# Performance work log

Hardware: AMD Instinct MI355X
Metric: run time of the kernel (lower is better)

## Reference

```python
import jax, jax.numpy as jnp
import numpy as np

K = 16

def _knn_idx(pts, k):
    # pts: [B, 3, N] -> idx [B, N, k] (self-inclusive nearest neighbors)
    inner = -2.0 * jnp.einsum('bdn,bdm->bnm', pts, pts)
    xx = jnp.sum(pts * pts, axis=1)  # [B, N]
    pd = -xx[:, :, None] - inner - xx[:, None, :]  # negative squared distance
    _, idx = jax.lax.top_k(pd, k)
    return idx

def _gather(feats, idx):
    # feats: [B, N, D], idx: [B, N, k] -> [B, N, k, D]
    return jax.vmap(lambda f, i: f[i])(feats, idx)

def _conv1x1(x, w, b):
    # x: [B, Cin, N], w: [Cout, Cin], b: [Cout]
    return jnp.einsum('oi,bin->bon', w, x) + b[None, :, None]

def _linear(x, w, b):
    # x: [B, N, Din], w: [Dout, Din]
    return jnp.einsum('bnd,od->bno', x, w) + b

def _local_cov(pts, idx):
    # pts: [B, 3, N] -> [B, 12, N]
    nb = _gather(jnp.swapaxes(pts, 1, 2), idx)  # [B, N, k, 3]
    outer = nb[:, :, 0, :, None] * nb[:, :, 1, None, :]  # [B, N, 3, 3]
    B, N = pts.shape[0], pts.shape[2]
    outer = jnp.swapaxes(outer.reshape(B, N, 9), 1, 2)  # [B, 9, N]
    return jnp.concatenate([pts, outer], axis=1)

def _local_maxpool(x, idx):
    # x: [B, D, N] -> [B, N, D]
    nb = _gather(jnp.swapaxes(x, 1, 2), idx)  # [B, N, k, D]
    return jnp.max(nb, axis=2)

def setup_inputs() -> dict:
    key = jax.random.key(0)
    ks = jax.random.split(key, 20)
    def w(k, shape):
        return jax.random.normal(k, shape, dtype=jnp.float32) * 0.05
    pts = jax.random.normal(ks[0], (8, 3, 4096), dtype=jnp.float32)
    return {
        'pts': pts,
        'm1w1': w(ks[1], (64, 12)), 'm1b1': w(ks[2], (64,)),
        'm1w2': w(ks[3], (64, 64)), 'm1b2': w(ks[4], (64,)),
        'm1w3': w(ks[5], (64, 64)), 'm1b3': w(ks[6], (64,)),
        'l1w': w(ks[7], (64, 64)), 'l1b': w(ks[8], (64,)),
        'c1w': w(ks[9], (128, 64)), 'c1b': w(ks[10], (128,)),
        'l2w': w(ks[11], (128, 128)), 'l2b': w(ks[12], (128,)),
        'c2w': w(ks[13], (1024, 128)), 'c2b': w(ks[14], (1024,)),
        'm2w1': w(ks[15], (512, 1024)), 'm2b1': w(ks[16], (512,)),
        'm2w2': w(ks[17], (512, 512)), 'm2b2': w(ks[18], (512,)),
    }

def reference(pts, m1w1, m1b1, m1w2, m1b2, m1w3, m1b3, l1w, l1b,
              c1w, c1b, l2w, l2b, c2w, c2b, m2w1, m2b1, m2w2, m2b2):
    idx = _knn_idx(pts, K)  # [B, N, k]
    x = _local_cov(pts, idx)  # [B, 12, N]
    # mlp1: three 1x1 convs with ReLU
    x = jax.nn.relu(_conv1x1(x, m1w1, m1b1))
    x = jax.nn.relu(_conv1x1(x, m1w2, m1b2))
    x = jax.nn.relu(_conv1x1(x, m1w3, m1b3))  # [B, 64, N]
    # graph layer
    x = _local_maxpool(x, idx)          # [B, N, 64]
    x = _linear(x, l1w, l1b)            # [B, N, 64]
    x = jnp.swapaxes(x, 1, 2)           # [B, 64, N]
    x = jax.nn.relu(_conv1x1(x, c1w, c1b))  # [B, 128, N]
    x = _local_maxpool(x, idx)          # [B, N, 128]
    x = _linear(x, l2w, l2b)            # [B, N, 128]
    x = jnp.swapaxes(x, 1, 2)           # [B, 128, N]
    x = _conv1x1(x, c2w, c2b)           # [B, 1024, N]
    # global max pool
    x = jnp.max(x, axis=2, keepdims=True)  # [B, 1024, 1]
    # mlp2
    x = jax.nn.relu(_conv1x1(x, m2w1, m2b1))
    x = _conv1x1(x, m2w2, m2b2)  # [B, 512, 1]
    return x.reshape(-1, 512)
```

## Files before the change

kernel.cpp:

```cpp
#include <hip/hip_runtime.h>
#include <cfloat>

#define NBATCH 8
#define NPTS   4096
#define KNN    16
#define PPB    16
#define NSL    16
#define CAP    24

typedef unsigned short u16;
typedef unsigned int   u32;
typedef __attribute__((ext_vector_type(8))) short short8;
typedef __attribute__((ext_vector_type(4))) float f32x4;

__device__ __forceinline__ float relu_f(float x) { return x > 0.f ? x : 0.f; }

__device__ __forceinline__ u32 bf16_split_pack(float v)
{
    unsigned u = __float_as_uint(v);
    unsigned hb = (u + 0x7FFFu + ((u >> 16) & 1u)) >> 16;
    float hf = __uint_as_float(hb << 16);
    float l = v - hf;
    unsigned ul = __float_as_uint(l);
    unsigned lb = (ul + 0x7FFFu + ((ul >> 16) & 1u)) >> 16;
    return (hb << 16) | (lb & 0xFFFFu);
}

__device__ __forceinline__ void unpack8(uint4 a, uint4 b, short8& h, short8& l)
{
    union { unsigned u[4]; short8 s; } H, L;
    H.u[0] = __builtin_amdgcn_perm(a.y, a.x, 0x07060302);
    H.u[1] = __builtin_amdgcn_perm(a.w, a.z, 0x07060302);
    H.u[2] = __builtin_amdgcn_perm(b.y, b.x, 0x07060302);
    H.u[3] = __builtin_amdgcn_perm(b.w, b.z, 0x07060302);
    L.u[0] = __builtin_amdgcn_perm(a.y, a.x, 0x05040100);
    L.u[1] = __builtin_amdgcn_perm(a.w, a.z, 0x05040100);
    L.u[2] = __builtin_amdgcn_perm(b.y, b.x, 0x05040100);
    L.u[3] = __builtin_amdgcn_perm(b.w, b.z, 0x05040100);
    h = H.s; l = L.s;
}

__global__ __launch_bounds__(256)
void knn_kernel(const float* __restrict__ pts, int* __restrict__ idxout)
{
    __shared__ __align__(16) float4 tile[8 * 129];
    __shared__ float  kl[PPB * NSL * 8];
    __shared__ float  thr[PPB];
    __shared__ int    cnt[PPB];

    const int b = blockIdx.y, tid = threadIdx.x;
    const int ptl = tid >> 4, r = tid & 15;
    const int n = blockIdx.x * PPB + ptl;
    const float* pb = pts + (size_t)b * 3 * NPTS;

    const float sx = pb[n], sy = pb[NPTS + n], sz = pb[2 * NPTS + n];

    float k8[8];
#pragma unroll
    for (int s = 0; s < 8; ++s) k8[s] = -FLT_MAX;

    const float4* slice = tile + (r >> 1) * 129 + (r & 1) * 64;

    for (int t = 0; t < 4; ++t) {
        if (t) __syncthreads();
        for (int i = tid; i < 1024; i += 256) {
            int j = t * 1024 + i;
            float x = pb[j], y = pb[NPTS + j], z = pb[2 * NPTS + j];
            float xx = __fadd_rn(__fadd_rn(__fmul_rn(x, x), __fmul_rn(y, y)),
                                 __fmul_rn(z, z));
            tile[(i >> 7) * 129 + (i & 127)] = make_float4(x, y, z, xx);
        }
        __syncthreads();
#pragma unroll 8
        for (int ii = 0; ii < 64; ++ii) {
            float4 c = slice[ii];
            float dt = __fmaf_rn(sx, c.x, __fmaf_rn(sy, c.y, __fmul_rn(sz, c.z)));
            float pd = __fmaf_rn(2.f, dt, -c.w);
            float old0 = k8[0];
#pragma unroll
            for (int s = 7; s >= 1; --s)
                k8[s] = __builtin_amdgcn_fmed3f(k8[s - 1], k8[s], pd);
            k8[0] = fmaxf(old0, pd);
        }
    }

#pragma unroll
    for (int s = 0; s < 8; ++s) kl[(ptl * NSL + r) * 8 + s] = k8[s];
    __syncthreads();

    if (r == 0) {
        const float* L = kl + ptl * (NSL * 8);
        int p[NSL];
#pragma unroll
        for (int l = 0; l < NSL; ++l) p[l] = 0;
        float tv = 0.f;
        for (int o = 0; o < 16; ++o) {
            float best = -FLT_MAX; int bi = 0;
#pragma unroll
            for (int l = 0; l < NSL; ++l) {
                float v = (p[l] < 8) ? L[l * 8 + p[l]] : -FLT_MAX;
                if (v > best) { best = v; bi = l; }
            }
#pragma unroll
            for (int l = 0; l < NSL; ++l) p[l] += (l == bi);
            tv = best;
        }
        thr[ptl] = tv;
        cnt[ptl] = 0;
    }
    __syncthreads();
    const float myThr = thr[ptl];

    float* pv = kl;
    int*   pi = (int*)(kl + PPB * CAP);

    for (int tt = 0; tt < 4; ++tt) {
        int t = 3 - tt;
        if (tt) {
            __syncthreads();
            for (int i = tid; i < 1024; i += 256) {
                int j = t * 1024 + i;
                float x = pb[j], y = pb[NPTS + j], z = pb[2 * NPTS + j];
                float xx = __fadd_rn(__fadd_rn(__fmul_rn(x, x), __fmul_rn(y, y)),
                                     __fmul_rn(z, z));
                tile[(i >> 7) * 129 + (i & 127)] = make_float4(x, y, z, xx);
            }
            __syncthreads();
        }
#pragma unroll 8
        for (int ii = 0; ii < 64; ++ii) {
            float4 c = slice[ii];
            float dt = __fmaf_rn(sx, c.x, __fmaf_rn(sy, c.y, __fmul_rn(sz, c.z)));
            float pd = __fmaf_rn(2.f, dt, -c.w);
            if (pd >= myThr) {
                int pos = atomicAdd(&cnt[ptl], 1);
                if (pos < CAP) {
                    pv[ptl * CAP + pos] = pd;
                    pi[ptl * CAP + pos] = t * 1024 + r * 64 + ii;
                }
            }
        }
    }
    __syncthreads();

    if (tid < PPB) {
        const int np = blockIdx.x * PPB + tid;
        int* out = idxout + ((size_t)b * NPTS + np) * KNN;
        int c = cnt[tid];
        if (c <= CAP) {
            float* v  = pv + tid * CAP;
            int*   ix = pi + tid * CAP;
            for (int o = 0; o < 16; ++o) {
                int best = o;
                for (int q = o + 1; q < c; ++q) {
                    float vq = v[q], vb = v[best];
                    if (vq > vb || (vq == vb && ix[q] < ix[best])) best = q;
                }
                float tv = v[o]; v[o] = v[best]; v[best] = tv;
                int   ti = ix[o]; ix[o] = ix[best]; ix[best] = ti;
                out[o] = ix[o];
            }
        } else {
            float qx = pb[np], qy = pb[NPTS + np], qz = pb[2 * NPTS + np];
            float v16[16]; int i16[16];
#pragma unroll
            for (int s = 0; s < 16; ++s) { v16[s] = -FLT_MAX; i16[s] = 0; }
            for (int j = 0; j < NPTS; ++j) {
                float x = pb[j], y = pb[NPTS + j], z = pb[2 * NPTS + j];
                float xx = __fadd_rn(__fadd_rn(__fmul_rn(x, x), __fmul_rn(y, y)),
                                     __fmul_rn(z, z));
                float dt = __fmaf_rn(qx, x, __fmaf_rn(qy, y, __fmul_rn(qz, z)));
                float pd = __fmaf_rn(2.f, dt, -xx);
                if (pd > v16[15]) {
                    int s = 15;
                    while (s > 0 && pd > v16[s - 1]) {
                        v16[s] = v16[s - 1]; i16[s] = i16[s - 1]; --s;
                    }
                    v16[s] = pd; i16[s] = j;
                }
            }
            for (int o = 0; o < 16; ++o) out[o] = i16[o];
        }
    }
}

__global__ __launch_bounds__(256)
void cov_mlp1_kernel(const float* __restrict__ pts, const int* __restrict__ idx,
                     const float* __restrict__ w1, const float* __restrict__ b1,
                     const float* __restrict__ w2, const float* __restrict__ b2,
                     const float* __restrict__ w3, const float* __restrict__ b3,
                     float* __restrict__ h3out)
{
    __shared__ __align__(16) float cov[64 * 16];
    __shared__ __align__(16) float w1s[64 * 16];
    __shared__ __align__(16) float w2s[64 * 68];
    __shared__ __align__(16) float w3s[64 * 68];
    __shared__ __align__(16) float hA[64 * 68];
    __shared__ __align__(16) float hB[64 * 68];

    const int b = blockIdx.y, tid = threadIdx.x;
    const int n0 = blockIdx.x * 64;
    const int pq = tid >> 4, cq = tid & 15;

    for (int i = tid; i < 64 * 4; i += 256) {
        int p = i >> 2, k4 = i & 3;
        float4 v = make_float4(0.f, 0.f, 0.f, 0.f);
        if (k4 < 3) v = *(const float4*)(w1 + p * 12 + k4 * 4);
        ((float4*)(w1s + p * 16))[k4] = v;
    }
    for (int i = tid; i < 64 * 16; i += 256) {
        int p = i >> 4, k4 = i & 15;
        ((float4*)(w2s + p * 68))[k4] = ((const float4*)(w2 + p * 64))[k4];
        ((float4*)(w3s + p * 68))[k4] = ((const float4*)(w3 + p * 64))[k4];
    }
    if (tid < 64) {
        const int n = n0 + tid;
        const int* ip = idx + ((size_t)b * NPTS + n) * KNN;
        int j0 = ip[0], j1 = ip[1];
        const float* pb = pts + (size_t)b * 3 * NPTS;
        float px = pb[n],  py = pb[NPTS + n],  pz = pb[2 * NPTS + n];
        float ax = pb[j0], ay = pb[NPTS + j0], az = pb[2 * NPTS + j0];
        float bx = pb[j1], by = pb[NPTS + j1], bz = pb[2 * NPTS + j1];
        float* cv = cov + tid * 16;
        cv[0] = px; cv[1] = py; cv[2] = pz;
        cv[3] = ax * bx; cv[4]  = ax * by; cv[5]  = ax * bz;
        cv[6] = ay * bx; cv[7]  = ay * by; cv[8]  = ay * bz;
        cv[9] = az * bx; cv[10] = az * by; cv[11] = az * bz;
        cv[12] = 0.f; cv[13] = 0.f; cv[14] = 0.f; cv[15] = 0.f;
    }
    __syncthreads();

    {
        float acc[4][4];
#pragma unroll
        for (int i = 0; i < 4; ++i)
#pragma unroll
            for (int j = 0; j < 4; ++j) acc[i][j] = 0.f;
        const float4* X4 = (const float4*)cov;
        const float4* W4 = (const float4*)w1s;
#pragma unroll
        for (int k4 = 0; k4 < 4; ++k4) {
            float4 xa[4], wb[4];
#pragma unroll
            for (int i = 0; i < 4; ++i) xa[i] = X4[(pq * 4 + i) * 4 + k4];
#pragma unroll
            for (int j = 0; j < 4; ++j) wb[j] = W4[(cq + 16 * j) * 4 + k4];
#pragma unroll
            for (int i = 0; i < 4; ++i)
#pragma unroll
                for (int j = 0; j < 4; ++j)
                    acc[i][j] += xa[i].x * wb[j].x + xa[i].y * wb[j].y
                               + xa[i].z * wb[j].z + xa[i].w * wb[j].w;
        }
#pragma unroll
        for (int j = 0; j < 4; ++j) {
            int c = cq + 16 * j;
            float bias = b1[c];
#pragma unroll
            for (int i = 0; i < 4; ++i)
                hA[(pq * 4 + i) * 68 + c] = relu_f(acc[i][j] + bias);
        }
    }
    __syncthreads();

    {
        float acc[4][4];
#pragma unroll
        for (int i = 0; i < 4; ++i)
#pragma unroll
            for (int j = 0; j < 4; ++j) acc[i][j] = 0.f;
        const float4* X4 = (const float4*)hA;
        const float4* W4 = (const float4*)w2s;
        for (int k4 = 0; k4 < 16; ++k4) {
            float4 xa[4], wb[4];
#pragma unroll
            for (int i = 0; i < 4; ++i) xa[i] = X4[(pq * 4 + i) * 17 + k4];
#pragma unroll
            for (int j = 0; j < 4; ++j) wb[j] = W4[(cq + 16 * j) * 17 + k4];
#pragma unroll
            for (int i = 0; i < 4; ++i)
#pragma unroll
                for (int j = 0; j < 4; ++j)
                    acc[i][j] += xa[i].x * wb[j].x + xa[i].y * wb[j].y
                               + xa[i].z * wb[j].z + xa[i].w * wb[j].w;
        }
#pragma unroll
        for (int j = 0; j < 4; ++j) {
            int c = cq + 16 * j;
            float bias = b2[c];
#pragma unroll
            for (int i = 0; i < 4; ++i)
                hB[(pq * 4 + i) * 68 + c] = relu_f(acc[i][j] + bias);
        }
    }
    __syncthreads();

    {
        float acc[4][4];
#pragma unroll
        for (int i = 0; i < 4; ++i)
#pragma unroll
            for (int j = 0; j < 4; ++j) acc[i][j] = 0.f;
        const float4* X4 = (const float4*)hB;
        const float4* W4 = (const float4*)w3s;
        for (int k4 = 0; k4 < 16; ++k4) {
            float4 xa[4], wb[4];
#pragma unroll
            for (int i = 0; i < 4; ++i) xa[i] = X4[(pq * 4 + i) * 17 + k4];
#pragma unroll
            for (int j = 0; j < 4; ++j) wb[j] = W4[(cq + 16 * j) * 17 + k4];
#pragma unroll
            for (int i = 0; i < 4; ++i)
#pragma unroll
                for (int j = 0; j < 4; ++j)
                    acc[i][j] += xa[i].x * wb[j].x + xa[i].y * wb[j].y
                               + xa[i].z * wb[j].z + xa[i].w * wb[j].w;
        }
#pragma unroll
        for (int j = 0; j < 4; ++j) {
            int c = cq + 16 * j;
            float bias = b3[c];
#pragma unroll
            for (int i = 0; i < 4; ++i)
                h3out[((size_t)b * NPTS + n0 + pq * 4 + i) * 64 + c] =
                    relu_f(acc[i][j] + bias);
        }
    }
}

template <int DV4>
__global__ __launch_bounds__(256)
void maxpool4_kernel(const float4* __restrict__ f, const int* __restrict__ idx,
                     float4* __restrict__ out)
{
    constexpr int SH = (DV4 == 16) ? 4 : 5;
    int t = blockIdx.x * 256 + threadIdx.x;
    int d4 = t & (DV4 - 1);
    int n  = (t >> SH) & (NPTS - 1);
    int b  = t >> (SH + 12);
    const int* ip = idx + ((size_t)b * NPTS + n) * KNN;
    const float4* fb = f + (size_t)b * NPTS * DV4;
    float4 v = make_float4(-FLT_MAX, -FLT_MAX, -FLT_MAX, -FLT_MAX);
#pragma unroll
    for (int k = 0; k < KNN; ++k) {
        float4 c = fb[(size_t)ip[k] * DV4 + d4];
        v.x = fmaxf(v.x, c.x); v.y = fmaxf(v.y, c.y);
        v.z = fmaxf(v.z, c.z); v.w = fmaxf(v.w, c.w);
    }
    out[t] = v;
}

__global__ __launch_bounds__(256)
void lin_conv1_kernel(const float* __restrict__ xin,
                      const float* __restrict__ l1w, const float* __restrict__ l1b,
                      const float* __restrict__ c1w, const float* __restrict__ c1b,
                      float* __restrict__ yout)
{
    __shared__ __align__(16) float sx[64 * 68];
    __shared__ __align__(16) float wbuf[64 * 68];
    __shared__ __align__(16) float t1[64 * 68];
    const int b = blockIdx.y, tid = threadIdx.x;
    const int n0 = blockIdx.x * 64;
    const int pq = tid >> 4, cq = tid & 15;

    for (int i = tid; i < 64 * 16; i += 256) {
        int p = i >> 4, k4 = i & 15;
        ((float4*)(sx + p * 68))[k4] =
            ((const float4*)(xin + ((size_t)b * NPTS + n0 + p) * 64))[k4];
        ((float4*)(wbuf + p * 68))[k4] = ((const float4*)(l1w + p * 64))[k4];
    }
    __syncthreads();

    {
        float acc[4][4];
#pragma unroll
        for (int i = 0; i < 4; ++i)
#pragma unroll
            for (int j = 0; j < 4; ++j) acc[i][j] = 0.f;
        const float4* X4 = (const float4*)sx;
        const float4* W4 = (const float4*)wbuf;
        for (int k4 = 0; k4 < 16; ++k4) {
            float4 xa[4], wb[4];
#pragma unroll
            for (int i = 0; i < 4; ++i) xa[i] = X4[(pq * 4 + i) * 17 + k4];
#pragma unroll
            for (int j = 0; j < 4; ++j) wb[j] = W4[(cq + 16 * j) * 17 + k4];
#pragma unroll
            for (int i = 0; i < 4; ++i)
#pragma unroll
                for (int j = 0; j < 4; ++j)
                    acc[i][j] += xa[i].x * wb[j].x + xa[i].y * wb[j].y
                               + xa[i].z * wb[j].z + xa[i].w * wb[j].w;
        }
#pragma unroll
        for (int j = 0; j < 4; ++j) {
            int c = cq + 16 * j;
            float bias = l1b[c];
#pragma unroll
            for (int i = 0; i < 4; ++i)
                t1[(pq * 4 + i) * 68 + c] = acc[i][j] + bias;
        }
    }

    for (int g = 0; g < 2; ++g) {
        __syncthreads();
        for (int i = tid; i < 64 * 16; i += 256) {
            int p = i >> 4, k4 = i & 15;
            ((float4*)(wbuf + p * 68))[k4] =
                ((const float4*)(c1w + (size_t)(g * 64 + p) * 64))[k4];
        }
        __syncthreads();
        float acc[4][4];
#pragma unroll
        for (int i = 0; i < 4; ++i)
#pragma unroll
            for (int j = 0; j < 4; ++j) acc[i][j] = 0.f;
        const float4* X4 = (const float4*)t1;
        const float4* W4 = (const float4*)wbuf;
        for (int k4 = 0; k4 < 16; ++k4) {
            float4 xa[4], wb[4];
#pragma unroll
            for (int i = 0; i < 4; ++i) xa[i] = X4[(pq * 4 + i) * 17 + k4];
#pragma unroll
            for (int j = 0; j < 4; ++j) wb[j] = W4[(cq + 16 * j) * 17 + k4];
#pragma unroll
            for (int i = 0; i < 4; ++i)
#pragma unroll
                for (int j = 0; j < 4; ++j)
                    acc[i][j] += xa[i].x * wb[j].x + xa[i].y * wb[j].y
                               + xa[i].z * wb[j].z + xa[i].w * wb[j].w;
        }
#pragma unroll
        for (int j = 0; j < 4; ++j) {
            int c = g * 64 + cq + 16 * j;
            float bias = c1b[c];
#pragma unroll
            for (int i = 0; i < 4; ++i)
                yout[((size_t)b * NPTS + n0 + pq * 4 + i) * 128 + c] =
                    relu_f(acc[i][j] + bias);
        }
    }
}

__global__ __launch_bounds__(256)
void lin2_kernel(const float* __restrict__ xin, const float* __restrict__ w,
                 const float* __restrict__ bias, u32* __restrict__ xpk)
{
    __shared__ __align__(16) float Xs[64 * 132];
    __shared__ __align__(16) float Ws[64 * 132];
    const int chunk = blockIdx.x, g = blockIdx.y, b = blockIdx.z;
    const int tid = threadIdx.x;

    for (int i = tid; i < 64 * 32; i += 256) {
        int p = i >> 5, k4 = i & 31;
        ((float4*)(Xs + p * 132))[k4] =
            ((const float4*)(xin + ((size_t)b * NPTS + chunk * 64 + p) * 128))[k4];
        ((float4*)(Ws + p * 132))[k4] =
            ((const float4*)(w + (size_t)(g * 64 + p) * 128))[k4];
    }
    __syncthreads();

    const int pq = tid >> 4, cq = tid & 15;
    const float4* X4 = (const float4*)Xs;
    const float4* W4 = (const float4*)Ws;
    float acc[4][4];
#pragma unroll
    for (int i = 0; i < 4; ++i)
#pragma unroll
        for (int j = 0; j < 4; ++j) acc[i][j] = 0.f;

    for (int k4 = 0; k4 < 32; ++k4) {
        float4 xa[4], wb[4];
#pragma unroll
        for (int i = 0; i < 4; ++i) xa[i] = X4[(pq * 4 + i) * 33 + k4];
#pragma unroll
        for (int j = 0; j < 4; ++j) wb[j] = W4[(cq + 16 * j) * 33 + k4];
#pragma unroll
        for (int i = 0; i < 4; ++i)
#pragma unroll
            for (int j = 0; j < 4; ++j)
                acc[i][j] += xa[i].x * wb[j].x + xa[i].y * wb[j].y
                           + xa[i].z * wb[j].z + xa[i].w * wb[j].w;
    }
#pragma unroll
    for (int j = 0; j < 4; ++j) {
        int c = g * 64 + cq + 16 * j;
        float bv = bias[c];
#pragma unroll
        for (int i = 0; i < 4; ++i) {
            float v = acc[i][j] + bv;
            size_t oidx = ((size_t)b * NPTS + chunk * 64 + pq * 4 + i) * 128 + c;
            xpk[oidx] = bf16_split_pack(v);
        }
    }
}

__global__ __launch_bounds__(256)
void wsplit_kernel(const float* __restrict__ w, u32* __restrict__ wpk)
{
    int t = blockIdx.x * 256 + threadIdx.x;
    wpk[t] = bf16_split_pack(w[t]);
}

__global__ __launch_bounds__(256)
void conv2max_mfma(const u32* __restrict__ xpk, const u32* __restrict__ wpk,
                   const float* __restrict__ bias, float* __restrict__ pmax)
{
    __shared__ __align__(16) u16 lds[4 * 16384];
    u16* Wh = lds;
    u16* Wl = lds + 16384;
    u16* Xh = lds + 2 * 16384;
    u16* Xl = lds + 3 * 16384;

    const int chunk = blockIdx.x, g = blockIdx.y, b = blockIdx.z;
    const int tid = threadIdx.x;
    const int lane = tid & 63, wave = tid >> 6;
    const int l15 = lane & 15, l4 = lane >> 4;
    const int wm = wave >> 1, wn = wave & 1;

    const u32* wp_g = wpk + (size_t)g * 128 * 128;
    const u32* xp_g = xpk + ((size_t)b * NPTS + chunk * 128) * 128;

    for (int u = tid; u < 2048; u += 256) {
        int row = u & 127, seg = u >> 7;
        int go = row * 128 + seg * 8;
        int lo_ = seg * 1024 + row * 8;
        uint4 a = *(const uint4*)&wp_g[go];
        uint4 b4 = *(const uint4*)&wp_g[go + 4];
        short8 h, l;
        unpack8(a, b4, h, l);
        *(short8*)&Wh[lo_] = h; *(short8*)&Wl[lo_] = l;
        a = *(const uint4*)&xp_g[go];
        b4 = *(const uint4*)&xp_g[go + 4];
        unpack8(a, b4, h, l);
        *(short8*)&Xh[lo_] = h; *(short8*)&Xl[lo_] = l;
    }
    __syncthreads();

    f32x4 acc[4][4];
#pragma unroll
    for (int mt = 0; mt < 4; ++mt)
#pragma unroll
        for (int nt = 0; nt < 4; ++nt)
            acc[mt][nt] = (f32x4){0.f, 0.f, 0.f, 0.f};

    for (int kb = 0; kb < 4; ++kb) {
        const int seg = kb * 4 + l4;
        short8 Ah[4], Al[4], Bh[4], Bl[4];
#pragma unroll
        for (int mt = 0; mt < 4; ++mt) {
            int off = seg * 1024 + (wm * 64 + mt * 16 + l15) * 8;
            Ah[mt] = *(const short8*)&Wh[off];
            Al[mt] = *(const short8*)&Wl[off];
        }
#pragma unroll
        for (int nt = 0; nt < 4; ++nt) {
            int off = seg * 1024 + (wn * 64 + nt * 16 + l15) * 8;
            Bh[nt] = *(const short8*)&Xh[off];
            Bl[nt] = *(const short8*)&Xl[off];
        }
#pragma unroll
        for (int mt = 0; mt < 4; ++mt)
#pragma unroll
            for (int nt = 0; nt < 4; ++nt) {
                acc[mt][nt] = __builtin_amdgcn_mfma_f32_16x16x32_bf16(
                    Ah[mt], Bh[nt], acc[mt][nt], 0, 0, 0);
                acc[mt][nt] = __builtin_amdgcn_mfma_f32_16x16x32_bf16(
                    Ah[mt], Bl[nt], acc[mt][nt], 0, 0, 0);
                acc[mt][nt] = __builtin_amdgcn_mfma_f32_16x16x32_bf16(
                    Al[mt], Bh[nt], acc[mt][nt], 0, 0, 0);
            }
    }

    __syncthreads();
    float* smax = (float*)lds;
#pragma unroll
    for (int mt = 0; mt < 4; ++mt)
#pragma unroll
        for (int r = 0; r < 4; ++r) {
            float m = fmaxf(fmaxf(acc[mt][0][r], acc[mt][1][r]),
                            fmaxf(acc[mt][2][r], acc[mt][3][r]));
            int c = wm * 64 + mt * 16 + 4 * l4 + r;
            smax[c * 33 + wn * 16 + l15] = m;
        }
    __syncthreads();
    if (tid < 128) {
        const float* row = smax + tid * 33;
        float v = row[0];
#pragma unroll
        for (int j = 1; j < 32; ++j) v = fmaxf(v, row[j]);
        int c = g * 128 + tid;
        pmax[((size_t)b * 32 + chunk) * 1024 + c] = v + bias[c];
    }
}

__global__ __launch_bounds__(256)
void gmax_kernel(const float* __restrict__ pmax, float* __restrict__ gmax)
{
    int t = blockIdx.x * 256 + threadIdx.x;
    int b = t >> 10, ch = t & 1023;
    const float* pp = pmax + (size_t)b * 32 * 1024 + ch;
    float v = -FLT_MAX;
    for (int c = 0; c < 32; ++c) v = fmaxf(v, pp[c * 1024]);
    gmax[t] = v;
}

__global__ __launch_bounds__(128)
void mlp2a_kernel(const float* __restrict__ g, const float* __restrict__ w1,
                  const float* __restrict__ b1, float* __restrict__ h)
{
    __shared__ __align__(16) float sg[1024];
    const int b = blockIdx.y, tid = threadIdx.x;
    for (int i = tid; i < 1024; i += 128) sg[i] = g[b * 1024 + i];
    __syncthreads();
    const int ch = blockIdx.x * 128 + tid;
    const float4* xr = (const float4*)sg;
    const float4* wr = (const float4*)(w1 + (size_t)ch * 1024);
    float a0 = 0.f, a1 = 0.f, a2 = 0.f, a3 = 0.f;
    for (int k = 0; k < 256; ++k) {
        float4 w = wr[k], x = xr[k];
        a0 += w.x * x.x; a1 += w.y * x.y; a2 += w.z * x.z; a3 += w.w * x.w;
    }
    h[b * 512 + ch] = relu_f(b1[ch] + ((a0 + a1) + (a2 + a3)));
}

__global__ __launch_bounds__(128)
void mlp2b_kernel(const float* __restrict__ h, const float* __restrict__ w2,
                  const float* __restrict__ b2, float* __restrict__ out)
{
    __shared__ __align__(16) float sh[512];
    const int b = blockIdx.y, tid = threadIdx.x;
    for (int i = tid; i < 512; i += 128) sh[i] = h[b * 512 + i];
    __syncthreads();
    const int ch = blockIdx.x * 128 + tid;
    const float4* xr = (const float4*)sh;
    const float4* wr = (const float4*)(w2 + (size_t)ch * 512);
    float a0 = 0.f, a1 = 0.f, a2 = 0.f, a3 = 0.f;
    for (int k = 0; k < 128; ++k) {
        float4 w = wr[k], x = xr[k];
        a0 += w.x * x.x; a1 += w.y * x.y; a2 += w.z * x.z; a3 += w.w * x.w;
    }
    out[b * 512 + ch] = b2[ch] + ((a0 + a1) + (a2 + a3));
}

extern "C" void kernel_launch(void* const* d_in, const int* in_sizes, int n_in,
                              void* d_out, int out_size, void* d_ws, size_t ws_size,
                              hipStream_t stream)
{
    const float* pts  = (const float*)d_in[0];
    const float* m1w1 = (const float*)d_in[1];
    const float* m1b1 = (const float*)d_in[2];
    const float* m1w2 = (const float*)d_in[3];
    const float* m1b2 = (const float*)d_in[4];
    const float* m1w3 = (const float*)d_in[5];
    const float* m1b3 = (const float*)d_in[6];
    const float* l1w  = (const float*)d_in[7];
    const float* l1b  = (const float*)d_in[8];
    const float* c1w  = (const float*)d_in[9];
    const float* c1b  = (const float*)d_in[10];
    const float* l2w  = (const float*)d_in[11];
    const float* l2b  = (const float*)d_in[12];
    const float* c2w  = (const float*)d_in[13];
    const float* c2b  = (const float*)d_in[14];
    const float* m2w1 = (const float*)d_in[15];
    const float* m2b1 = (const float*)d_in[16];
    const float* m2w2 = (const float*)d_in[17];
    const float* m2b2 = (const float*)d_in[18];

    char* ws = (char*)d_ws;
    size_t off = 0;
    int*   idx   = (int*)(ws + off);   off += (size_t)NBATCH * NPTS * KNN * 4;
    float* h3    = (float*)(ws + off); off += (size_t)NBATCH * NPTS * 64 * 4;
    float* mp1   = (float*)(ws + off); off += (size_t)NBATCH * NPTS * 64 * 4;
    float* y1    = (float*)(ws + off); off += (size_t)NBATCH * NPTS * 128 * 4;
    float* mp2   = (float*)(ws + off); off += (size_t)NBATCH * NPTS * 128 * 4;
    float* pmaxb = (float*)(ws + off); off += (size_t)NBATCH * 64 * 1024 * 4;
    float* gmx   = (float*)(ws + off); off += (size_t)NBATCH * 1024 * 4;
    float* hbuf  = (float*)(ws + off); off += (size_t)NBATCH * 512 * 4;
    u32*   wpk   = (u32*)(ws + off);   off += (size_t)1024 * 128 * 4;
    u32*   xpk   = (u32*)y1;

    wsplit_kernel<<<dim3(512), 256, 0, stream>>>(c2w, wpk);
    knn_kernel<<<dim3(NPTS / PPB, NBATCH), 256, 0, stream>>>(pts, idx);
    cov_mlp1_kernel<<<dim3(64, NBATCH), 256, 0, stream>>>(pts, idx, m1w1, m1b1,
                                                          m1w2, m1b2, m1w3, m1b3, h3);
    maxpool4_kernel<16><<<dim3(NBATCH * NPTS * 16 / 256), 256, 0, stream>>>(
        (const float4*)h3, idx, (float4*)mp1);
    lin_conv1_kernel<<<dim3(64, NBATCH), 256, 0, stream>>>(mp1, l1w, l1b, c1w, c1b, y1);
    maxpool4_kernel<32><<<dim3(NBATCH * NPTS * 32 / 256), 256, 0, stream>>>(
        (const float4*)y1, idx, (float4*)mp2);
    lin2_kernel<<<dim3(64, 2, NBATCH), 256, 0, stream>>>(mp2, l2w, l2b, xpk);
    conv2max_mfma<<<dim3(32, 8, NBATCH), 256, 0, stream>>>(xpk, wpk, c2b, pmaxb);
    gmax_kernel<<<dim3(32), 256, 0, stream>>>(pmaxb, gmx);
    mlp2a_kernel<<<dim3(4, NBATCH), 128, 0, stream>>>(gmx, m2w1, m2b1, hbuf);
    mlp2b_kernel<<<dim3(4, NBATCH), 128, 0, stream>>>(hbuf, m2w2, m2b2, (float*)d_out);
}
```

Baseline: 333.3 us.

## Process 32 query points per KNN block with 8 candidate slices each

Doubles the number of query points per block and halves the number of threads per query, so each thread scans 128 candidates per tile instead of 64. Each loaded candidate tile is reused by more queries, and the final top-16 merge runs over 8 sorted lists instead of 16, written as an unrolled max-reduction. In exchange each thread does a longer serial insertion chain and the grid has half as many blocks. The tie-breaking order of the merge also changes.

```diff
diff --git a/kernel.cpp b/kernel.cpp
--- a/kernel.cpp
+++ b/kernel.cpp
@@ -4,8 +4,8 @@
 #define NBATCH 8
 #define NPTS   4096
 #define KNN    16
-#define PPB    16
-#define NSL    16
+#define PPB    32
+#define NSL    8
 #define CAP    24
 
 typedef unsigned short u16;
@@ -43,13 +43,13 @@
 __global__ __launch_bounds__(256)
 void knn_kernel(const float* __restrict__ pts, int* __restrict__ idxout)
 {
-    __shared__ __align__(16) float4 tile[8 * 129];
+    __shared__ __align__(16) float4 tile[NSL * 129];
     __shared__ float  kl[PPB * NSL * 8];
     __shared__ float  thr[PPB];
     __shared__ int    cnt[PPB];
 
     const int b = blockIdx.y, tid = threadIdx.x;
-    const int ptl = tid >> 4, r = tid & 15;
+    const int ptl = tid >> 3, r = tid & 7;
     const int n = blockIdx.x * PPB + ptl;
     const float* pb = pts + (size_t)b * 3 * NPTS;
 
@@ -59,7 +59,7 @@
 #pragma unroll
     for (int s = 0; s < 8; ++s) k8[s] = -FLT_MAX;
 
-    const float4* slice = tile + (r >> 1) * 129 + (r & 1) * 64;
+    const float4* slice = tile + r * 129;
 
     for (int t = 0; t < 4; ++t) {
         if (t) __syncthreads();
@@ -72,7 +72,7 @@
         }
         __syncthreads();
 #pragma unroll 8
-        for (int ii = 0; ii < 64; ++ii) {
+        for (int ii = 0; ii < 128; ++ii) {
             float4 c = slice[ii];
             float dt = __fmaf_rn(sx, c.x, __fmaf_rn(sy, c.y, __fmul_rn(sz, c.z)));
             float pd = __fmaf_rn(2.f, dt, -c.w);
@@ -89,21 +89,29 @@
     __syncthreads();
 
     if (r == 0) {
-        const float* L = kl + ptl * (NSL * 8);
-        int p[NSL];
-#pragma unroll
-        for (int l = 0; l < NSL; ++l) p[l] = 0;
+        const float* L = kl + ptl * 64;
+        int p0 = 0, p1 = 0, p2 = 0, p3 = 0, p4 = 0, p5 = 0, p6 = 0, p7 = 0;
         float tv = 0.f;
         for (int o = 0; o < 16; ++o) {
-            float best = -FLT_MAX; int bi = 0;
-#pragma unroll
-            for (int l = 0; l < NSL; ++l) {
-                float v = (p[l] < 8) ? L[l * 8 + p[l]] : -FLT_MAX;
-                if (v > best) { best = v; bi = l; }
-            }
-#pragma unroll
-            for (int l = 0; l < NSL; ++l) p[l] += (l == bi);
-            tv = best;
+            float v0 = (p0 < 8) ? L[p0]      : -FLT_MAX;
+            float v1 = (p1 < 8) ? L[8 + p1]  : -FLT_MAX;
+            float v2 = (p2 < 8) ? L[16 + p2] : -FLT_MAX;
+            float v3 = (p3 < 8) ? L[24 + p3] : -FLT_MAX;
+            float v4 = (p4 < 8) ? L[32 + p4] : -FLT_MAX;
+            float v5 = (p5 < 8) ? L[40 + p5] : -FLT_MAX;
+            float v6 = (p6 < 8) ? L[48 + p6] : -FLT_MAX;
+            float v7 = (p7 < 8) ? L[56 + p7] : -FLT_MAX;
+            float m = fmaxf(fmaxf(fmaxf(v0, v1), fmaxf(v2, v3)),
+                            fmaxf(fmaxf(v4, v5), fmaxf(v6, v7)));
+            tv = m;
+            if      (v0 == m) ++p0;
+            else if (v1 == m) ++p1;
+            else if (v2 == m) ++p2;
+            else if (v3 == m) ++p3;
+            else if (v4 == m) ++p4;
+            else if (v5 == m) ++p5;
+            else if (v6 == m) ++p6;
+            else              ++p7;
         }
         thr[ptl] = tv;
         cnt[ptl] = 0;
@@ -128,7 +136,7 @@
             __syncthreads();
         }
 #pragma unroll 8
-        for (int ii = 0; ii < 64; ++ii) {
+        for (int ii = 0; ii < 128; ++ii) {
             float4 c = slice[ii];
             float dt = __fmaf_rn(sx, c.x, __fmaf_rn(sy, c.y, __fmul_rn(sz, c.z)));
             float pd = __fmaf_rn(2.f, dt, -c.w);
@@ -136,7 +144,7 @@
                 int pos = atomicAdd(&cnt[ptl], 1);
                 if (pos < CAP) {
                     pv[ptl * CAP + pos] = pd;
-                    pi[ptl * CAP + pos] = t * 1024 + r * 64 + ii;
+                    pi[ptl * CAP + pos] = t * 1024 + r * 128 + ii;
                 }
             }
         }
```

Result: faster. 299.0 us (-10.3%).
